# Kernel tuning notes

Measured on AMD Instinct MI355X. Metric: run time of the kernel, lower is better.

The kernel has to match this reference:

```python
import jax, jax.numpy as jnp
import numpy as np

N = 100000      # nodes
E = 1_600_000   # edges
IN = 128        # in_channels
HID = 32        # hidden_channels (per head)
HEADS = 4
NC = 10         # num_classes
NEG_SLOPE = 0.2 # GATConv leaky relu slope
BN_EPS = 1e-5


def _gat_conv(x, src, dst, W, a_src, a_dst, bias, heads, out_ch, concat):
    # x: [N, F_in]; W: [F_in, heads*out_ch]; a_src/a_dst: [heads, out_ch]
    n = x.shape[0]
    h = (x @ W).reshape(n, heads, out_ch)                    # [N,H,C]
    al_src = jnp.sum(h * a_src, axis=-1)                     # [N,H]
    al_dst = jnp.sum(h * a_dst, axis=-1)                     # [N,H]
    e = jax.nn.leaky_relu(al_src[src] + al_dst[dst], NEG_SLOPE)  # [E,H]
    # segment softmax over destination node
    m = jax.ops.segment_max(e, dst, num_segments=n)          # [N,H]
    ex = jnp.exp(e - m[dst])
    s = jax.ops.segment_sum(ex, dst, num_segments=n)         # [N,H]
    alpha = ex / (s[dst] + 1e-16)                            # [E,H]
    out = jax.ops.segment_sum(h[src] * alpha[:, :, None], dst, num_segments=n)  # [N,H,C]
    if concat:
        out = out.reshape(n, heads * out_ch)
    else:
        out = out.mean(axis=1)
    return out + bias


def _bn(x, gamma, beta, mean, var):
    # eval-mode BatchNorm1d with running stats
    return (x - mean) * jax.lax.rsqrt(var + BN_EPS) * gamma + beta


def setup_inputs() -> dict:
    key = jax.random.key(0)
    ks = iter(jax.random.split(key, 40))
    d = {}
    d['x'] = jax.random.normal(next(ks), (N, IN), dtype=jnp.float32)
    d['edge_index'] = jax.random.randint(next(ks), (2, E), 0, N, dtype=jnp.int32)
    dims = [(IN, HID, HEADS), (HID * HEADS, HID, HEADS), (HID * HEADS, HID, 1)]
    for i, (fin, c, h) in enumerate(dims):
        d[f'W{i}'] = jax.random.normal(next(ks), (fin, h * c), dtype=jnp.float32) * (1.0 / np.sqrt(fin))
        d[f'as{i}'] = jax.random.normal(next(ks), (h, c), dtype=jnp.float32) * 0.1
        d[f'ad{i}'] = jax.random.normal(next(ks), (h, c), dtype=jnp.float32) * 0.1
        bdim = h * c if i < 2 else c
        d[f'b{i}'] = jnp.zeros((bdim,), dtype=jnp.float32)
        d[f'g{i}'] = jax.random.uniform(next(ks), (bdim,), dtype=jnp.float32, minval=0.5, maxval=1.5)
        d[f'bt{i}'] = jax.random.normal(next(ks), (bdim,), dtype=jnp.float32) * 0.1
        d[f'm{i}'] = jax.random.normal(next(ks), (bdim,), dtype=jnp.float32) * 0.1
        d[f'v{i}'] = jax.random.uniform(next(ks), (bdim,), dtype=jnp.float32, minval=0.5, maxval=1.5)
    d['Wc'] = jax.random.normal(next(ks), (HID, NC), dtype=jnp.float32) * (1.0 / np.sqrt(HID))
    d['bc'] = jnp.zeros((NC,), dtype=jnp.float32)
    return d


def reference(x, edge_index, W0, as0, ad0, b0, g0, bt0, m0, v0,
              W1, as1, ad1, b1, g1, bt1, m1, v1,
              W2, as2, ad2, b2, g2, bt2, m2, v2, Wc, bc):
    src, dst = edge_index[0], edge_index[1]
    # layer 0: concat heads
    h = _gat_conv(x, src, dst, W0, as0, ad0, b0, HEADS, HID, True)
    h = jax.nn.elu(_bn(h, g0, bt0, m0, v0))
    # layer 1: concat heads
    h = _gat_conv(h, src, dst, W1, as1, ad1, b1, HEADS, HID, True)
    h = jax.nn.elu(_bn(h, g1, bt1, m1, v1))
    # layer 2: single head, no concat
    h = _gat_conv(h, src, dst, W2, as2, ad2, b2, 1, HID, False)
    h = jax.nn.elu(_bn(h, g2, bt2, m2, v2))
    # dropout is identity in eval mode
    return h @ Wc + bc
```

## Files before the change

### kernel.cpp

```cpp
#include <hip/hip_runtime.h>
#include <hip/hip_bf16.h>
#include <math.h>

#define NN   100000
#define NE   1600000
#define FIN  128
#define HID  32
#define NHEADS 4
#define NCLS 10

typedef unsigned int uint32;
typedef __fp16 half2_t __attribute__((ext_vector_type(2)));
typedef __fp16 half8_t __attribute__((ext_vector_type(8)));
typedef float  f32x4   __attribute__((ext_vector_type(4)));

__device__ __forceinline__ uint32 packh2(float a, float b) {
    half2_t h = __builtin_amdgcn_cvt_pkrtz(a, b);
    return __builtin_bit_cast(uint32, h);
}
__device__ __forceinline__ float h_lo(uint32 v) {
    return (float)__builtin_bit_cast(half2_t, v)[0];
}
__device__ __forceinline__ float h_hi(uint32 v) {
    return (float)__builtin_bit_cast(half2_t, v)[1];
}
__device__ __forceinline__ half8_t as_h8(uint4 v) {
    return __builtin_bit_cast(half8_t, v);
}

__global__ void zero_i32(int* __restrict__ p, int n) {
    int i = blockIdx.x * blockDim.x + threadIdx.x;
    if (i < n) p[i] = 0;
}

__global__ void hist_rank_kernel(const int* __restrict__ dst, int* __restrict__ cnt,
                                 int* __restrict__ rank, int e) {
    const int t0 = blockIdx.x * (blockDim.x * 4) + threadIdx.x;
    int d[4];
    bool a[4];
#pragma unroll
    for (int k = 0; k < 4; ++k) {
        const int j = t0 + k * 256;
        a[k] = (j < e);
        d[k] = a[k] ? dst[j] : 0;
    }
    int r[4];
#pragma unroll
    for (int k = 0; k < 4; ++k)
        if (a[k]) r[k] = atomicAdd(&cnt[d[k]], 1);
#pragma unroll
    for (int k = 0; k < 4; ++k) {
        const int j = t0 + k * 256;
        if (a[k]) rank[j] = r[k];
    }
}

__global__ void scan_block_sums(const int* __restrict__ cnt, int* __restrict__ bsum, int n) {
    __shared__ int sm[256];
    int i = blockIdx.x * 256 + threadIdx.x;
    int v = (i < n) ? cnt[i] : 0;
    sm[threadIdx.x] = v;
    __syncthreads();
    for (int off = 128; off > 0; off >>= 1) {
        if (threadIdx.x < off) sm[threadIdx.x] += sm[threadIdx.x + off];
        __syncthreads();
    }
    if (threadIdx.x == 0) bsum[blockIdx.x] = sm[0];
}

__global__ void scan_single(const int* __restrict__ bsum, int* __restrict__ boff, int nb) {
    __shared__ int sm[512];
    int t = threadIdx.x;
    int v = (t < nb) ? bsum[t] : 0;
    sm[t] = v;
    __syncthreads();
    for (int off = 1; off < 512; off <<= 1) {
        int u = (t >= off) ? sm[t - off] : 0;
        __syncthreads();
        sm[t] += u;
        __syncthreads();
    }
    if (t < nb) boff[t] = sm[t] - v;
}

__global__ void scan_final(const int* __restrict__ cnt, const int* __restrict__ boff,
                           int* __restrict__ rowptr, int n) {
    __shared__ int sm[256];
    int i = blockIdx.x * 256 + threadIdx.x;
    int v = (i < n) ? cnt[i] : 0;
    sm[threadIdx.x] = v;
    __syncthreads();
    for (int off = 1; off < 256; off <<= 1) {
        int u = (threadIdx.x >= off) ? sm[threadIdx.x - off] : 0;
        __syncthreads();
        sm[threadIdx.x] += u;
        __syncthreads();
    }
    int incl = sm[threadIdx.x];
    int excl = incl - v;
    if (i < n) rowptr[i] = boff[blockIdx.x] + excl;
    if (i == n - 1) rowptr[n] = boff[blockIdx.x] + incl;
}

__global__ void scatter_kernel(const int* __restrict__ src, const int* __restrict__ dst,
                               const int* __restrict__ rank, const int* __restrict__ rowptr,
                               int* __restrict__ esrc, int e) {
    const int t0 = blockIdx.x * (blockDim.x * 4) + threadIdx.x;
#pragma unroll
    for (int k = 0; k < 4; ++k) {
        const int j = t0 + k * 256;
        if (j < e) {
            const int d = dst[j];
            esrc[rowptr[d] + rank[j]] = src[j];
        }
    }
}

__global__ void conv_x_kernel(const float* __restrict__ x, uint32* __restrict__ Xh, int n4) {
    int i = blockIdx.x * blockDim.x + threadIdx.x;
    if (i >= n4) return;
    const float4 v = ((const float4*)x)[i];
    ((uint2*)Xh)[i] = make_uint2(packh2(v.x, v.y), packh2(v.z, v.w));
}

__global__ void conv_w_kernel(const float* __restrict__ W0, const float* __restrict__ W1,
                              const float* __restrict__ W2, uint32* __restrict__ Wt0,
                              uint32* __restrict__ Wt1, uint32* __restrict__ Wt2) {
    int t = blockIdx.x * blockDim.x + threadIdx.x;
    if (t < 8192) {
        const int nn = t >> 6, ku = t & 63;
        Wt0[t] = packh2(W0[(2 * ku) * 128 + nn], W0[(2 * ku + 1) * 128 + nn]);
    } else if (t < 16384) {
        const int l = t - 8192;
        const int nn = l >> 6, ku = l & 63;
        Wt1[l] = packh2(W1[(2 * ku) * 128 + nn], W1[(2 * ku + 1) * 128 + nn]);
    } else if (t < 18432) {
        const int l = t - 16384;
        const int nn = l >> 6, ku = l & 63;
        Wt2[l] = packh2(W2[(2 * ku) * 32 + nn], W2[(2 * ku + 1) * 32 + nn]);
    }
}

template <int FOUT, int H>
__global__ __launch_bounds__(256) void gemm_mfma(const uint32* __restrict__ Xh,
                                                 const uint32* __restrict__ Wt,
                                                 const float* __restrict__ a_s,
                                                 const float* __restrict__ a_d,
                                                 float* __restrict__ alS,
                                                 float* __restrict__ alD,
                                                 uint32* __restrict__ Outh, int n) {
    constexpr int NT = FOUT / 16;
    const int wave = threadIdx.x >> 6;
    const int lane = threadIdx.x & 63;
    const int c = lane & 15;
    const int q = lane >> 4;
    const int row0 = blockIdx.x * 128 + wave * 32;

    int r0 = row0 + c;
    int r1 = row0 + 16 + c;
    if (r0 >= n) r0 = n - 1;
    if (r1 >= n) r1 = n - 1;

    f32x4 acc[2][NT];
#pragma unroll
    for (int m = 0; m < 2; ++m)
#pragma unroll
        for (int nt = 0; nt < NT; ++nt) acc[m][nt] = (f32x4){0.f, 0.f, 0.f, 0.f};

    const uint4* XU = (const uint4*)Xh;
    const uint4* WU = (const uint4*)Wt;

#pragma unroll
    for (int ks = 0; ks < 4; ++ks) {
        const half8_t a0 = as_h8(XU[(size_t)r0 * 16 + ks * 4 + q]);
        const half8_t a1 = as_h8(XU[(size_t)r1 * 16 + ks * 4 + q]);
#pragma unroll
        for (int nt = 0; nt < NT; ++nt) {
            const half8_t b = as_h8(WU[(nt * 16 + c) * 16 + ks * 4 + q]);
            acc[0][nt] = __builtin_amdgcn_mfma_f32_16x16x32_f16(a0, b, acc[0][nt], 0, 0, 0);
            acc[1][nt] = __builtin_amdgcn_mfma_f32_16x16x32_f16(a1, b, acc[1][nt], 0, 0, 0);
        }
    }

    float asv[NT], adv[NT];
#pragma unroll
    for (int nt = 0; nt < NT; ++nt) {
        asv[nt] = a_s[c + 16 * nt];
        adv[nt] = a_d[c + 16 * nt];
    }

#pragma unroll
    for (int m = 0; m < 2; ++m) {
#pragma unroll
        for (int reg = 0; reg < 4; ++reg) {
            const int grow = row0 + m * 16 + q * 4 + reg;
            const bool ok = (grow < n);
            if constexpr (H == 4) {
                float ps[4], pd[4];
#pragma unroll
                for (int h = 0; h < 4; ++h) {
                    ps[h] = acc[m][2 * h][reg] * asv[2 * h] + acc[m][2 * h + 1][reg] * asv[2 * h + 1];
                    pd[h] = acc[m][2 * h][reg] * adv[2 * h] + acc[m][2 * h + 1][reg] * adv[2 * h + 1];
                }
#pragma unroll
                for (int off = 1; off < 16; off <<= 1) {
#pragma unroll
                    for (int h = 0; h < 4; ++h) {
                        ps[h] += __shfl_xor(ps[h], off);
                        pd[h] += __shfl_xor(pd[h], off);
                    }
                }
                if (c < 4 && ok) {
                    const float vs = (c == 0) ? ps[0] : (c == 1) ? ps[1] : (c == 2) ? ps[2] : ps[3];
                    const float vd = (c == 0) ? pd[0] : (c == 1) ? pd[1] : (c == 2) ? pd[2] : pd[3];
                    alS[(size_t)grow * 4 + c] = vs;
                    alD[(size_t)grow * 4 + c] = vd;
                }
            } else {
                float ps = acc[m][0][reg] * asv[0] + acc[m][1][reg] * asv[1];
                float pd = acc[m][0][reg] * adv[0] + acc[m][1][reg] * adv[1];
#pragma unroll
                for (int off = 1; off < 16; off <<= 1) {
                    ps += __shfl_xor(ps, off);
                    pd += __shfl_xor(pd, off);
                }
                if (c == 0 && ok) {
                    alS[grow] = ps;
                    alD[grow] = pd;
                }
            }
#pragma unroll
            for (int nt = 0; nt < NT; ++nt) {
                const float v = acc[m][nt][reg];
                const float o = __shfl_xor(v, 1);
                if (((c & 1) == 0) && ok) {
                    Outh[(size_t)grow * (FOUT / 2) + nt * 8 + (c >> 1)] = packh2(v, o);
                }
            }
        }
    }
}

template <int H, int C>
__global__ __launch_bounds__(256) void gat_aggregate(
    const uint32* __restrict__ Hb,
    const int* __restrict__ rowptr, const int* __restrict__ esrc,
    const float* __restrict__ alS, const float* __restrict__ alD,
    const float* __restrict__ bias, const float* __restrict__ gamma,
    const float* __restrict__ beta, const float* __restrict__ bnmean,
    const float* __restrict__ bnvar, uint32* __restrict__ B16, int n) {
    constexpr int F  = H * C;
    constexpr int RW = F / 2;
    constexpr int NW = 4;
    __shared__ __align__(16) int   s_src[NW][68];
    __shared__ __align__(16) float s_ex[NW][H][68];

    const int wave = threadIdx.x >> 6;
    const int lane = threadIdx.x & 63;
    const int d    = blockIdx.x * NW + wave;
    if (d >= n) return;

    if (lane < 4) {
        s_src[wave][64 + lane] = 0;
#pragma unroll
        for (int h = 0; h < H; ++h) s_ex[wave][h][64 + lane] = 0.f;
    }
    __builtin_amdgcn_wave_barrier();

    const int beg = rowptr[d], end = rowptr[d + 1];
    float al_d[H], sl[H];
#pragma unroll
    for (int h = 0; h < H; ++h) {
        al_d[h] = alD[(size_t)d * H + h];
        sl[h]   = 0.f;
    }
    float acc0 = 0.f, acc1 = 0.f;
    const int head = (H == 4) ? (lane >> 4) : 0;

    for (int base = beg; base < end; base += 64) {
        const int j   = base + lane;
        const bool act = (j < end);
        int sj = 0;
        float ex[H];
        if (act) {
            sj = esrc[j];
            if constexpr (H == 4) {
                float4 av = *(const float4*)(alS + (size_t)sj * 4);
                float t0 = av.x + al_d[0], t1 = av.y + al_d[1];
                float t2 = av.z + al_d[2], t3 = av.w + al_d[3];
                t0 = t0 > 0.f ? t0 : 0.2f * t0;
                t1 = t1 > 0.f ? t1 : 0.2f * t1;
                t2 = t2 > 0.f ? t2 : 0.2f * t2;
                t3 = t3 > 0.f ? t3 : 0.2f * t3;
                ex[0] = __expf(t0); ex[1] = __expf(t1);
                ex[2] = __expf(t2); ex[3] = __expf(t3);
            } else {
                float t0 = alS[sj] + al_d[0];
                t0 = t0 > 0.f ? t0 : 0.2f * t0;
                ex[0] = __expf(t0);
            }
        } else {
#pragma unroll
            for (int h = 0; h < H; ++h) ex[h] = 0.f;
        }
#pragma unroll
        for (int h = 0; h < H; ++h) {
            s_ex[wave][h][lane] = ex[h];
            sl[h] += ex[h];
        }
        s_src[wave][lane] = sj;
        __builtin_amdgcn_wave_barrier();

        const int cc = min(64, end - base);
        if constexpr (H == 4) {
            const int ccr = (cc + 7) & ~7;
            for (int jj = 0; jj < ccr; jj += 8) {
                const int4   sa = *(const int4*)  &s_src[wave][jj];
                const int4   sb = *(const int4*)  &s_src[wave][jj + 4];
                const float4 wa = *(const float4*)&s_ex[wave][head][jj];
                const float4 wb = *(const float4*)&s_ex[wave][head][jj + 4];
                const int b0 = __builtin_amdgcn_readfirstlane(sa.x);
                const int b1 = __builtin_amdgcn_readfirstlane(sa.y);
                const int b2 = __builtin_amdgcn_readfirstlane(sa.z);
                const int b3 = __builtin_amdgcn_readfirstlane(sa.w);
                const int b4 = __builtin_amdgcn_readfirstlane(sb.x);
                const int b5 = __builtin_amdgcn_readfirstlane(sb.y);
                const int b6 = __builtin_amdgcn_readfirstlane(sb.z);
                const int b7 = __builtin_amdgcn_readfirstlane(sb.w);
                const uint32 v0 = Hb[(size_t)b0 * RW + lane];
                const uint32 v1 = Hb[(size_t)b1 * RW + lane];
                const uint32 v2 = Hb[(size_t)b2 * RW + lane];
                const uint32 v3 = Hb[(size_t)b3 * RW + lane];
                const uint32 v4 = Hb[(size_t)b4 * RW + lane];
                const uint32 v5 = Hb[(size_t)b5 * RW + lane];
                const uint32 v6 = Hb[(size_t)b6 * RW + lane];
                const uint32 v7 = Hb[(size_t)b7 * RW + lane];
                acc0 = fmaf(h_lo(v0), wa.x, acc0); acc1 = fmaf(h_hi(v0), wa.x, acc1);
                acc0 = fmaf(h_lo(v1), wa.y, acc0); acc1 = fmaf(h_hi(v1), wa.y, acc1);
                acc0 = fmaf(h_lo(v2), wa.z, acc0); acc1 = fmaf(h_hi(v2), wa.z, acc1);
                acc0 = fmaf(h_lo(v3), wa.w, acc0); acc1 = fmaf(h_hi(v3), wa.w, acc1);
                acc0 = fmaf(h_lo(v4), wb.x, acc0); acc1 = fmaf(h_hi(v4), wb.x, acc1);
                acc0 = fmaf(h_lo(v5), wb.y, acc0); acc1 = fmaf(h_hi(v5), wb.y, acc1);
                acc0 = fmaf(h_lo(v6), wb.z, acc0); acc1 = fmaf(h_hi(v6), wb.z, acc1);
                acc0 = fmaf(h_lo(v7), wb.w, acc0); acc1 = fmaf(h_hi(v7), wb.w, acc1);
            }
        } else {
            const int g  = lane >> 4;
            const int li = lane & 15;
            for (int jj = 0; jj < cc; jj += 4) {
                const int   idx = jj + g;
                const int   sj2 = s_src[wave][idx];
                const float w   = s_ex[wave][0][idx];
                const uint32 v  = Hb[(size_t)sj2 * RW + li];
                acc0 = fmaf(h_lo(v), w, acc0);
                acc1 = fmaf(h_hi(v), w, acc1);
            }
        }
        __builtin_amdgcn_wave_barrier();
    }

#pragma unroll
    for (int h = 0; h < H; ++h) {
#pragma unroll
        for (int off = 32; off > 0; off >>= 1) sl[h] += __shfl_xor(sl[h], off);
    }
    float sh;
    if constexpr (H == 4) {
        float a = (head & 1) ? sl[1] : sl[0];
        float b = (head & 1) ? sl[3] : sl[2];
        sh = (head & 2) ? b : a;
    } else {
        sh = sl[0];
        acc0 += __shfl_xor(acc0, 16); acc0 += __shfl_xor(acc0, 32);
        acc1 += __shfl_xor(acc1, 16); acc1 += __shfl_xor(acc1, 32);
    }

    const float inv = 1.f / (sh + 1e-16f);
    const int li  = (F == 128) ? lane : (lane & 15);
    const int c0 = 2 * li, c1 = 2 * li + 1;
    const bool wr = (F == 128) || (lane < 16);
    if (wr) {
        float o0 = acc0 * inv, o1 = acc1 * inv;
        float y0 = (o0 + bias[c0] - bnmean[c0]) * rsqrtf(bnvar[c0] + 1e-5f) * gamma[c0] + beta[c0];
        float y1 = (o1 + bias[c1] - bnmean[c1]) * rsqrtf(bnvar[c1] + 1e-5f) * gamma[c1] + beta[c1];
        y0 = y0 > 0.f ? y0 : expm1f(y0);
        y1 = y1 > 0.f ? y1 : expm1f(y1);
        B16[(size_t)d * RW + li] = packh2(y0, y1);
    }
}

__global__ void classifier_kernel(const uint32* __restrict__ H3, const float* __restrict__ Wc,
                                  const float* __restrict__ bc, float* __restrict__ out, int n) {
    int t  = blockIdx.x * blockDim.x + threadIdx.x;
    int ni = t / NCLS, c = t % NCLS;
    if (ni >= n) return;
    const uint32* row = H3 + (size_t)ni * 16;
    float a = bc[c];
#pragma unroll
    for (int u = 0; u < 16; ++u) {
        const uint32 v = row[u];
        a = fmaf(h_lo(v), Wc[(2 * u) * NCLS + c], a);
        a = fmaf(h_hi(v), Wc[(2 * u + 1) * NCLS + c], a);
    }
    out[(size_t)ni * NCLS + c] = a;
}

static inline char* align256(char* p) {
    return (char*)(((uintptr_t)p + 255) & ~(uintptr_t)255);
}

extern "C" void kernel_launch(void* const* d_in, const int* in_sizes, int n_in,
                              void* d_out, int out_size, void* d_ws, size_t ws_size,
                              hipStream_t stream) {
    const float* x  = (const float*)d_in[0];
    const int*   ei = (const int*)d_in[1];
    const int N = in_sizes[0] / FIN;
    const int E = in_sizes[1] / 2;
    const int* src = ei;
    const int* dst = ei + E;

    const float *W0 = (const float*)d_in[2],  *as0 = (const float*)d_in[3],
                *ad0 = (const float*)d_in[4], *b0 = (const float*)d_in[5],
                *g0 = (const float*)d_in[6],  *bt0 = (const float*)d_in[7],
                *m0 = (const float*)d_in[8],  *v0 = (const float*)d_in[9];
    const float *W1 = (const float*)d_in[10], *as1 = (const float*)d_in[11],
                *ad1 = (const float*)d_in[12],*b1 = (const float*)d_in[13],
                *g1 = (const float*)d_in[14], *bt1 = (const float*)d_in[15],
                *m1 = (const float*)d_in[16], *v1 = (const float*)d_in[17];
    const float *W2 = (const float*)d_in[18], *as2 = (const float*)d_in[19],
                *ad2 = (const float*)d_in[20],*b2 = (const float*)d_in[21],
                *g2 = (const float*)d_in[22], *bt2 = (const float*)d_in[23],
                *m2 = (const float*)d_in[24], *v2 = (const float*)d_in[25];
    const float *Wc = (const float*)d_in[26], *bc = (const float*)d_in[27];
    float* out = (float*)d_out;

    char* p = (char*)d_ws;
    uint32* Xh  = (uint32*)p;   p = align256(p + (size_t)N * 64 * 4);
    uint32* Ht  = (uint32*)p;   p = align256(p + (size_t)N * 64 * 4);
    uint32* B16 = (uint32*)p;   p = align256(p + (size_t)N * 64 * 4);
    uint32* Wt0 = (uint32*)p;   p = align256(p + 8192 * 4);
    uint32* Wt1 = (uint32*)p;   p = align256(p + 8192 * 4);
    uint32* Wt2 = (uint32*)p;   p = align256(p + 2048 * 4);
    float* alS = (float*)p;     p = align256(p + (size_t)N * NHEADS * 4);
    float* alD = (float*)p;     p = align256(p + (size_t)N * NHEADS * 4);
    int* cnt = (int*)p;         p = align256(p + (size_t)N * 4);
    int* rowptr = (int*)p;      p = align256(p + (size_t)(N + 1) * 4);
    int* rank = (int*)p;        p = align256(p + (size_t)E * 4);
    int* esrc = (int*)p;        p = align256(p + (size_t)E * 4);
    int* bsum = (int*)p;        p = align256(p + 512 * 4);
    int* boff = (int*)p;        p = align256(p + 512 * 4);
    (void)ws_size; (void)n_in; (void)out_size;

    const int NB = (N + 255) / 256;
    const int EB4 = (E + 1023) / 1024;

    zero_i32<<<NB, 256, 0, stream>>>(cnt, N);
    hist_rank_kernel<<<EB4, 256, 0, stream>>>(dst, cnt, rank, E);
    scan_block_sums<<<NB, 256, 0, stream>>>(cnt, bsum, N);
    scan_single<<<1, 512, 0, stream>>>(bsum, boff, NB);
    scan_final<<<NB, 256, 0, stream>>>(cnt, boff, rowptr, N);
    scatter_kernel<<<EB4, 256, 0, stream>>>(src, dst, rank, rowptr, esrc, E);

    conv_x_kernel<<<(N * 32 + 255) / 256, 256, 0, stream>>>(x, Xh, N * 32);
    conv_w_kernel<<<72, 256, 0, stream>>>(W0, W1, W2, Wt0, Wt1, Wt2);

    const int GB = (N + 127) / 128;
    const int AB = (N + 3) / 4;

    gemm_mfma<128, 4><<<GB, 256, 0, stream>>>(Xh, Wt0, as0, ad0, alS, alD, Ht, N);
    gat_aggregate<4, 32><<<AB, 256, 0, stream>>>(Ht, rowptr, esrc, alS, alD,
                                                 b0, g0, bt0, m0, v0, B16, N);
    gemm_mfma<128, 4><<<GB, 256, 0, stream>>>(B16, Wt1, as1, ad1, alS, alD, Ht, N);
    gat_aggregate<4, 32><<<AB, 256, 0, stream>>>(Ht, rowptr, esrc, alS, alD,
                                                 b1, g1, bt1, m1, v1, B16, N);
    gemm_mfma<32, 1><<<GB, 256, 0, stream>>>(B16, Wt2, as2, ad2, alS, alD, Ht, N);
    gat_aggregate<1, 32><<<AB, 256, 0, stream>>>(Ht, rowptr, esrc, alS, alD,
                                                 b2, g2, bt2, m2, v2, B16, N);
    classifier_kernel<<<(N * NCLS + 255) / 256, 256, 0, stream>>>(B16, Wc, bc, out, N);
}
```

Measured before the change: 551.7 us.

## Process two destination nodes per wave in GAT aggregation for memory-level parallelism

Each wave now handles two destination nodes at once, interleaving their edge chunks so the per-edge score gathers and the feature gathers for both nodes are issued together. The aim is more outstanding memory requests per wave to hide gather latency, with half as many blocks launched. The cost is more registers and shared memory per wave, which may lower occupancy. When the two nodes have different degrees, the wave idles on the shorter one while the longer one finishes.

```diff
diff --git a/kernel.cpp b/kernel.cpp
--- a/kernel.cpp
+++ b/kernel.cpp
@@ -252,140 +252,178 @@
     constexpr int F  = H * C;
     constexpr int RW = F / 2;
     constexpr int NW = 4;
-    __shared__ __align__(16) int   s_src[NW][68];
-    __shared__ __align__(16) float s_ex[NW][H][68];
+    __shared__ __align__(16) int   s_src[NW][2][68];
+    __shared__ __align__(16) float s_ex[NW][2][H][68];
 
     const int wave = threadIdx.x >> 6;
     const int lane = threadIdx.x & 63;
-    const int d    = blockIdx.x * NW + wave;
-    if (d >= n) return;
+    const int d0   = blockIdx.x * (NW * 2) + wave * 2;
 
     if (lane < 4) {
-        s_src[wave][64 + lane] = 0;
-#pragma unroll
-        for (int h = 0; h < H; ++h) s_ex[wave][h][64 + lane] = 0.f;
+#pragma unroll
+        for (int pp = 0; pp < 2; ++pp) {
+            s_src[wave][pp][64 + lane] = 0;
+#pragma unroll
+            for (int h = 0; h < H; ++h) s_ex[wave][pp][h][64 + lane] = 0.f;
+        }
     }
     __builtin_amdgcn_wave_barrier();
 
-    const int beg = rowptr[d], end = rowptr[d + 1];
-    float al_d[H], sl[H];
-#pragma unroll
-    for (int h = 0; h < H; ++h) {
-        al_d[h] = alD[(size_t)d * H + h];
-        sl[h]   = 0.f;
-    }
-    float acc0 = 0.f, acc1 = 0.f;
+    int beg[2], end[2];
+    float al_d[2][H], sl[2][H];
+#pragma unroll
+    for (int pp = 0; pp < 2; ++pp) {
+        const int d = d0 + pp;
+        const bool v = (d < n);
+        beg[pp] = v ? rowptr[d] : 0;
+        end[pp] = v ? rowptr[d + 1] : 0;
+#pragma unroll
+        for (int h = 0; h < H; ++h) {
+            al_d[pp][h] = v ? alD[(size_t)d * H + h] : 0.f;
+            sl[pp][h]   = 0.f;
+        }
+    }
+    float acc[2][2] = {{0.f, 0.f}, {0.f, 0.f}};
     const int head = (H == 4) ? (lane >> 4) : 0;
-
-    for (int base = beg; base < end; base += 64) {
-        const int j   = base + lane;
-        const bool act = (j < end);
-        int sj = 0;
-        float ex[H];
-        if (act) {
-            sj = esrc[j];
-            if constexpr (H == 4) {
-                float4 av = *(const float4*)(alS + (size_t)sj * 4);
-                float t0 = av.x + al_d[0], t1 = av.y + al_d[1];
-                float t2 = av.z + al_d[2], t3 = av.w + al_d[3];
-                t0 = t0 > 0.f ? t0 : 0.2f * t0;
-                t1 = t1 > 0.f ? t1 : 0.2f * t1;
-                t2 = t2 > 0.f ? t2 : 0.2f * t2;
-                t3 = t3 > 0.f ? t3 : 0.2f * t3;
-                ex[0] = __expf(t0); ex[1] = __expf(t1);
-                ex[2] = __expf(t2); ex[3] = __expf(t3);
-            } else {
-                float t0 = alS[sj] + al_d[0];
-                t0 = t0 > 0.f ? t0 : 0.2f * t0;
-                ex[0] = __expf(t0);
+    int base[2] = {beg[0], beg[1]};
+
+    for (;;) {
+        const bool act0 = (base[0] < end[0]);
+        const bool act1 = (base[1] < end[1]);
+        if (!act0 && !act1) break;
+
+#pragma unroll
+        for (int pp = 0; pp < 2; ++pp) {
+            if (base[pp] < end[pp]) {
+                const int j   = base[pp] + lane;
+                const bool a  = (j < end[pp]);
+                int sj = 0;
+                float ex[H];
+                if (a) {
+                    sj = esrc[j];
+                    if constexpr (H == 4) {
+                        float4 av = *(const float4*)(alS + (size_t)sj * 4);
+                        float t0 = av.x + al_d[pp][0], t1 = av.y + al_d[pp][1];
+                        float t2 = av.z + al_d[pp][2], t3 = av.w + al_d[pp][3];
+                        t0 = t0 > 0.f ? t0 : 0.2f * t0;
+                        t1 = t1 > 0.f ? t1 : 0.2f * t1;
+                        t2 = t2 > 0.f ? t2 : 0.2f * t2;
+                        t3 = t3 > 0.f ? t3 : 0.2f * t3;
+                        ex[0] = __expf(t0); ex[1] = __expf(t1);
+                        ex[2] = __expf(t2); ex[3] = __expf(t3);
+                    } else {
+                        float t0 = alS[sj] + al_d[pp][0];
+                        t0 = t0 > 0.f ? t0 : 0.2f * t0;
+                        ex[0] = __expf(t0);
+                    }
+                } else {
+#pragma unroll
+                    for (int h = 0; h < H; ++h) ex[h] = 0.f;
+                }
+#pragma unroll
+                for (int h = 0; h < H; ++h) {
+                    s_ex[wave][pp][h][lane] = ex[h];
+                    sl[pp][h] += ex[h];
+                }
+                s_src[wave][pp][lane] = sj;
             }
+        }
+        __builtin_amdgcn_wave_barrier();
+
+#pragma unroll
+        for (int pp = 0; pp < 2; ++pp) {
+            if (base[pp] < end[pp]) {
+                const int cc = min(64, end[pp] - base[pp]);
+                if constexpr (H == 4) {
+                    const int ccr = (cc + 7) & ~7;
+                    for (int jj = 0; jj < ccr; jj += 8) {
+                        const int4   sa = *(const int4*)  &s_src[wave][pp][jj];
+                        const int4   sb = *(const int4*)  &s_src[wave][pp][jj + 4];
+                        const float4 wa = *(const float4*)&s_ex[wave][pp][head][jj];
+                        const float4 wb = *(const float4*)&s_ex[wave][pp][head][jj + 4];
+                        const int b0 = __builtin_amdgcn_readfirstlane(sa.x);
+                        const int b1 = __builtin_amdgcn_readfirstlane(sa.y);
+                        const int b2 = __builtin_amdgcn_readfirstlane(sa.z);
+                        const int b3 = __builtin_amdgcn_readfirstlane(sa.w);
+                        const int b4 = __builtin_amdgcn_readfirstlane(sb.x);
+                        const int b5 = __builtin_amdgcn_readfirstlane(sb.y);
+                        const int b6 = __builtin_amdgcn_readfirstlane(sb.z);
+                        const int b7 = __builtin_amdgcn_readfirstlane(sb.w);
+                        const uint32 v0 = Hb[(size_t)b0 * RW + lane];
+                        const uint32 v1 = Hb[(size_t)b1 * RW + lane];
+                        const uint32 v2 = Hb[(size_t)b2 * RW + lane];
+                        const uint32 v3 = Hb[(size_t)b3 * RW + lane];
+                        const uint32 v4 = Hb[(size_t)b4 * RW + lane];
+                        const uint32 v5 = Hb[(size_t)b5 * RW + lane];
+                        const uint32 v6 = Hb[(size_t)b6 * RW + lane];
+                        const uint32 v7 = Hb[(size_t)b7 * RW + lane];
+                        acc[pp][0] = fmaf(h_lo(v0), wa.x, acc[pp][0]);
+                        acc[pp][1] = fmaf(h_hi(v0), wa.x, acc[pp][1]);
+                        acc[pp][0] = fmaf(h_lo(v1), wa.y, acc[pp][0]);
+                        acc[pp][1] = fmaf(h_hi(v1), wa.y, acc[pp][1]);
+                        acc[pp][0] = fmaf(h_lo(v2), wa.z, acc[pp][0]);
+                        acc[pp][1] = fmaf(h_hi(v2), wa.z, acc[pp][1]);
+                        acc[pp][0] = fmaf(h_lo(v3), wa.w, acc[pp][0]);
+                        acc[pp][1] = fmaf(h_hi(v3), wa.w, acc[pp][1]);
+                        acc[pp][0] = fmaf(h_lo(v4), wb.x, acc[pp][0]);
+                        acc[pp][1] = fmaf(h_hi(v4), wb.x, acc[pp][1]);
+                        acc[pp][0] = fmaf(h_lo(v5), wb.y, acc[pp][0]);
+                        acc[pp][1] = fmaf(h_hi(v5), wb.y, acc[pp][1]);
+                        acc[pp][0] = fmaf(h_lo(v6), wb.z, acc[pp][0]);
+                        acc[pp][1] = fmaf(h_hi(v6), wb.z, acc[pp][1]);
+                        acc[pp][0] = fmaf(h_lo(v7), wb.w, acc[pp][0]);
+                        acc[pp][1] = fmaf(h_hi(v7), wb.w, acc[pp][1]);
+                    }
+                } else {
+                    const int g  = lane >> 4;
+                    const int li = lane & 15;
+                    for (int jj = 0; jj < cc; jj += 4) {
+                        const int   idx = jj + g;
+                        const int   sj2 = s_src[wave][pp][idx];
+                        const float w   = s_ex[wave][pp][0][idx];
+                        const uint32 v  = Hb[(size_t)sj2 * RW + li];
+                        acc[pp][0] = fmaf(h_lo(v), w, acc[pp][0]);
+                        acc[pp][1] = fmaf(h_hi(v), w, acc[pp][1]);
+                    }
+                }
+            }
+        }
+        __builtin_amdgcn_wave_barrier();
+        base[0] += 64;
+        base[1] += 64;
+    }
+
+#pragma unroll
+    for (int pp = 0; pp < 2; ++pp) {
+        const int d = d0 + pp;
+#pragma unroll
+        for (int h = 0; h < H; ++h) {
+#pragma unroll
+            for (int off = 32; off > 0; off >>= 1) sl[pp][h] += __shfl_xor(sl[pp][h], off);
+        }
+        float a0 = acc[pp][0], a1 = acc[pp][1];
+        float sh;
+        if constexpr (H == 4) {
+            float a = (head & 1) ? sl[pp][1] : sl[pp][0];
+            float b = (head & 1) ? sl[pp][3] : sl[pp][2];
+            sh = (head & 2) ? b : a;
         } else {
-#pragma unroll
-            for (int h = 0; h < H; ++h) ex[h] = 0.f;
-        }
-#pragma unroll
-        for (int h = 0; h < H; ++h) {
-            s_ex[wave][h][lane] = ex[h];
-            sl[h] += ex[h];
-        }
-        s_src[wave][lane] = sj;
-        __builtin_amdgcn_wave_barrier();
-
-        const int cc = min(64, end - base);
-        if constexpr (H == 4) {
-            const int ccr = (cc + 7) & ~7;
-            for (int jj = 0; jj < ccr; jj += 8) {
-                const int4   sa = *(const int4*)  &s_src[wave][jj];
-                const int4   sb = *(const int4*)  &s_src[wave][jj + 4];
-                const float4 wa = *(const float4*)&s_ex[wave][head][jj];
-                const float4 wb = *(const float4*)&s_ex[wave][head][jj + 4];
-                const int b0 = __builtin_amdgcn_readfirstlane(sa.x);
-                const int b1 = __builtin_amdgcn_readfirstlane(sa.y);
-                const int b2 = __builtin_amdgcn_readfirstlane(sa.z);
-                const int b3 = __builtin_amdgcn_readfirstlane(sa.w);
-                const int b4 = __builtin_amdgcn_readfirstlane(sb.x);
-                const int b5 = __builtin_amdgcn_readfirstlane(sb.y);
-                const int b6 = __builtin_amdgcn_readfirstlane(sb.z);
-                const int b7 = __builtin_amdgcn_readfirstlane(sb.w);
-                const uint32 v0 = Hb[(size_t)b0 * RW + lane];
-                const uint32 v1 = Hb[(size_t)b1 * RW + lane];
-                const uint32 v2 = Hb[(size_t)b2 * RW + lane];
-                const uint32 v3 = Hb[(size_t)b3 * RW + lane];
-                const uint32 v4 = Hb[(size_t)b4 * RW + lane];
-                const uint32 v5 = Hb[(size_t)b5 * RW + lane];
-                const uint32 v6 = Hb[(size_t)b6 * RW + lane];
-                const uint32 v7 = Hb[(size_t)b7 * RW + lane];
-                acc0 = fmaf(h_lo(v0), wa.x, acc0); acc1 = fmaf(h_hi(v0), wa.x, acc1);
-                acc0 = fmaf(h_lo(v1), wa.y, acc0); acc1 = fmaf(h_hi(v1), wa.y, acc1);
-                acc0 = fmaf(h_lo(v2), wa.z, acc0); acc1 = fmaf(h_hi(v2), wa.z, acc1);
-                acc0 = fmaf(h_lo(v3), wa.w, acc0); acc1 = fmaf(h_hi(v3), wa.w, acc1);
-                acc0 = fmaf(h_lo(v4), wb.x, acc0); acc1 = fmaf(h_hi(v4), wb.x, acc1);
-                acc0 = fmaf(h_lo(v5), wb.y, acc0); acc1 = fmaf(h_hi(v5), wb.y, acc1);
-                acc0 = fmaf(h_lo(v6), wb.z, acc0); acc1 = fmaf(h_hi(v6), wb.z, acc1);
-                acc0 = fmaf(h_lo(v7), wb.w, acc0); acc1 = fmaf(h_hi(v7), wb.w, acc1);
-            }
-        } else {
-            const int g  = lane >> 4;
-            const int li = lane & 15;
-            for (int jj = 0; jj < cc; jj += 4) {
-                const int   idx = jj + g;
-                const int   sj2 = s_src[wave][idx];
-                const float w   = s_ex[wave][0][idx];
-                const uint32 v  = Hb[(size_t)sj2 * RW + li];
-                acc0 = fmaf(h_lo(v), w, acc0);
-                acc1 = fmaf(h_hi(v), w, acc1);
-            }
-        }
-        __builtin_amdgcn_wave_barrier();
-    }
-
-#pragma unroll
-    for (int h = 0; h < H; ++h) {
-#pragma unroll
-        for (int off = 32; off > 0; off >>= 1) sl[h] += __shfl_xor(sl[h], off);
-    }
-    float sh;
-    if constexpr (H == 4) {
-        float a = (head & 1) ? sl[1] : sl[0];
-        float b = (head & 1) ? sl[3] : sl[2];
-        sh = (head & 2) ? b : a;
-    } else {
-        sh = sl[0];
-        acc0 += __shfl_xor(acc0, 16); acc0 += __shfl_xor(acc0, 32);
-        acc1 += __shfl_xor(acc1, 16); acc1 += __shfl_xor(acc1, 32);
-    }
-
-    const float inv = 1.f / (sh + 1e-16f);
-    const int li  = (F == 128) ? lane : (lane & 15);
-    const int c0 = 2 * li, c1 = 2 * li + 1;
-    const bool wr = (F == 128) || (lane < 16);
-    if (wr) {
-        float o0 = acc0 * inv, o1 = acc1 * inv;
-        float y0 = (o0 + bias[c0] - bnmean[c0]) * rsqrtf(bnvar[c0] + 1e-5f) * gamma[c0] + beta[c0];
-        float y1 = (o1 + bias[c1] - bnmean[c1]) * rsqrtf(bnvar[c1] + 1e-5f) * gamma[c1] + beta[c1];
-        y0 = y0 > 0.f ? y0 : expm1f(y0);
-        y1 = y1 > 0.f ? y1 : expm1f(y1);
-        B16[(size_t)d * RW + li] = packh2(y0, y1);
+            sh = sl[pp][0];
+            a0 += __shfl_xor(a0, 16); a0 += __shfl_xor(a0, 32);
+            a1 += __shfl_xor(a1, 16); a1 += __shfl_xor(a1, 32);
+        }
+        const float inv = 1.f / (sh + 1e-16f);
+        const int li  = (F == 128) ? lane : (lane & 15);
+        const int c0 = 2 * li, c1 = 2 * li + 1;
+        const bool wr = ((F == 128) || (lane < 16)) && (d < n);
+        if (wr) {
+            float o0 = a0 * inv, o1 = a1 * inv;
+            float y0 = (o0 + bias[c0] - bnmean[c0]) * rsqrtf(bnvar[c0] + 1e-5f) * gamma[c0] + beta[c0];
+            float y1 = (o1 + bias[c1] - bnmean[c1]) * rsqrtf(bnvar[c1] + 1e-5f) * gamma[c1] + beta[c1];
+            y0 = y0 > 0.f ? y0 : expm1f(y0);
+            y1 = y1 > 0.f ? y1 : expm1f(y1);
+            B16[(size_t)d * RW + li] = packh2(y0, y1);
+        }
     }
 }
 
@@ -465,7 +503,7 @@
     conv_w_kernel<<<72, 256, 0, stream>>>(W0, W1, W2, Wt0, Wt1, Wt2);
 
     const int GB = (N + 127) / 128;
-    const int AB = (N + 3) / 4;
+    const int AB = (N + 7) / 8;
 
     gemm_mfma<128, 4><<<GB, 256, 0, stream>>>(Xh, Wt0, as0, ad0, alS, alD, Ht, N);
     gat_aggregate<4, 32><<<AB, 256, 0, stream>>>(Ht, rowptr, esrc, alS, alD,
```

Result: slower. 576.1 us (+4.4%).
